# Performance work log

Measured on AMD Instinct MI355X. Metric: run time of the kernel, lower is better.

The kernel has to match this reference:

```python
import jax, jax.numpy as jnp
import numpy as np

B, CIN, H, W = 32, 256, 32, 32
DK, DV, HEADS, OUT = 128, 128, 8, 256
DKH = DK // HEADS
DVH = DV // HEADS


def _conv1x1(x, w, b):
    # x: [B,C,H,W], w: [O,C], b: [O]
    return jnp.einsum('bchw,oc->bohw', x, w) + b[None, :, None, None]


def setup_inputs() -> dict:
    key = jax.random.key(0)
    ks = jax.random.split(key, 7)
    s = 0.02
    return {
        'x': jax.random.normal(ks[0], (B, CIN, H, W), jnp.float32),
        'w_qkv': jax.random.normal(ks[1], (2 * DK + DV, CIN), jnp.float32) * s,
        'b_qkv': jnp.zeros((2 * DK + DV,), jnp.float32),
        'w_attn': jax.random.normal(ks[2], (DV, DV), jnp.float32) * s,
        'b_attn': jnp.zeros((DV,), jnp.float32),
        'w_out': jax.random.normal(ks[3], (OUT - DV, CIN), jnp.float32) * s,
        'b_out': jnp.zeros((OUT - DV,), jnp.float32),
    }


def reference(x, w_qkv, b_qkv, w_attn, b_attn, w_out, b_out):
    b = x.shape[0]
    N = H * W
    # parallel conv branch (kernel_size=1 so spatial dims match attention branch)
    conv_out = _conv1x1(x, w_out, b_out)  # [B, OUT-DV, H, W]
    # qkv projection
    qkv = _conv1x1(x, w_qkv, b_qkv)  # [B, 2*DK+DV, H, W]
    q, k, v = jnp.split(qkv, [DK, 2 * DK], axis=1)
    q = q.reshape(b, HEADS, DKH, N) * (DKH ** -0.5)
    k = k.reshape(b, HEADS, DKH, N)
    v = v.reshape(b, HEADS, DVH, N)
    # scaled dot-product attention over the N=H*W flattened positions
    logits = jnp.einsum('bhdq,bhdk->bhqk', q, k)  # [B,heads,N,N]
    weights = jax.nn.softmax(logits, axis=-1)
    attn = jnp.einsum('bhqk,bhdk->bhdq', weights, v)  # [B,heads,DVH,N]
    attn = attn.reshape(b, DV, H, W)
    attn = _conv1x1(attn, w_attn, b_attn)
    return jnp.concatenate([conv_out, attn], axis=1)
```

## Files before the change

kernel.cpp:

```cpp
#include <hip/hip_runtime.h>
#include <hip/hip_bf16.h>

#define BATCH 32
#define CIN   256
#define NPOS  1024
#define DKC   128
#define DVC   128
#define HEADS 8
#define OUTC  256

typedef __bf16 bf16x8 __attribute__((ext_vector_type(8)));
typedef __bf16 bf16x4 __attribute__((ext_vector_type(4)));
typedef float  f32x4  __attribute__((ext_vector_type(4)));
typedef float  f32x16 __attribute__((ext_vector_type(16)));
typedef unsigned u32x4 __attribute__((ext_vector_type(4)));

#define QSCALE 0.3606737602f

__device__ inline bf16x8 load8(const __bf16* p) {
    return *reinterpret_cast<const bf16x8*>(p);
}
__device__ inline f32x4 fzero4() {
    f32x4 z;
#pragma unroll
    for (int i = 0; i < 4; ++i) z[i] = 0.0f;
    return z;
}
__device__ inline float fexp2(float x) {
#if __has_builtin(__builtin_amdgcn_exp2f)
    return __builtin_amdgcn_exp2f(x);
#else
    return exp2f(x);
#endif
}

__global__ __launch_bounds__(256) void detect_dtype(const unsigned short* __restrict__ xraw,
                                                    int* __restrict__ flag) {
    __shared__ int s;
    if (threadIdx.x == 0) s = 0;
    __syncthreads();
    int cnt = 0;
#pragma unroll
    for (int j = 0; j < 64; ++j) {
        unsigned short u = xraw[threadIdx.x * 64 + j];
        unsigned int e = (u >> 7) & 0xFF;
        if (e >= 0x92) cnt++;
    }
    if (cnt) atomicAdd(&s, cnt);
    __syncthreads();
    if (threadIdx.x == 0) *flag = (s > 0) ? 1 : 0;
}

#define CV_WQKV 98304
#define CV_WOUT (CV_WQKV + 32768)
#define CV_BQKV (CV_WOUT + 384)
#define CV_BOUT (CV_BQKV + 128)
#define CV_WATT (CV_BOUT + 16384)
#define CV_BATT (CV_WATT + 128)
__global__ __launch_bounds__(256) void convert_all(
    const void* __restrict__ w_qkv, const void* __restrict__ b_qkv,
    const void* __restrict__ w_attn, const void* __restrict__ b_attn,
    const void* __restrict__ w_out, const void* __restrict__ b_out,
    __bf16* __restrict__ wcat, __bf16* __restrict__ bcat,
    __bf16* __restrict__ w_attnc, __bf16* __restrict__ b_attnc,
    const int* __restrict__ flag) {
    int i = blockIdx.x * 256 + threadIdx.x;
    const void* src; __bf16* dst; int j;
    if      (i < CV_WQKV) { src = w_qkv;  j = i;           dst = wcat + i; }
    else if (i < CV_WOUT) { src = w_out;  j = i - CV_WQKV; dst = wcat + i; }
    else if (i < CV_BQKV) { src = b_qkv;  j = i - CV_WOUT; dst = bcat + j; }
    else if (i < CV_BOUT) { src = b_out;  j = i - CV_BQKV; dst = bcat + 384 + j; }
    else if (i < CV_WATT) { src = w_attn; j = i - CV_BOUT; dst = w_attnc + j; }
    else if (i < CV_BATT) { src = b_attn; j = i - CV_WATT; dst = b_attnc + j; }
    else return;
    if (*flag) *dst = (__bf16)((const float*)src)[j];
    else       *dst = ((const __bf16*)src)[j];
}

__global__ __launch_bounds__(512, 4) void qkv_conv_gemm3(
    const void* __restrict__ xv,
    const __bf16* __restrict__ wcat,
    const __bf16* __restrict__ bcat,
    __bf16* __restrict__ q_ws,
    __bf16* __restrict__ k_ws,
    __bf16* __restrict__ v_ws,
    void* __restrict__ out,
    const int* __restrict__ flag)
{
    __shared__ __bf16 xs[64][264];
    bool isf32 = (*flag != 0);
    int b   = blockIdx.y;
    int n0  = blockIdx.x * 64;
    int t   = threadIdx.x;
    int nl  = t & 63, cb = t >> 6;

#pragma unroll
    for (int cs = 0; cs < 32; ++cs) {
        int c = cs * 8 + cb;
        size_t gi = ((size_t)b * CIN + c) * NPOS + n0 + nl;
        float v = isf32 ? ((const float*)xv)[gi] : (float)((const __bf16*)xv)[gi];
        xs[nl][c] = (__bf16)v;
    }
    __syncthreads();

    int wave = t >> 6;
    int lane = t & 63;
    int quad = lane >> 4, colid = lane & 15;
    int row0 = (wave >> 2) * 256 + (wave & 3) * 64;

    const __bf16* wp = wcat + (size_t)(row0 + colid) * CIN + quad * 8;

    f32x4 acc[4][4];
#pragma unroll
    for (int rt = 0; rt < 4; ++rt)
#pragma unroll
        for (int st = 0; st < 4; ++st) acc[rt][st] = fzero4();

#pragma unroll
    for (int k0 = 0; k0 < CIN; k0 += 32) {
        bf16x8 aA[4], bB[4];
#pragma unroll
        for (int rt = 0; rt < 4; ++rt)
            aA[rt] = load8(wp + (size_t)rt * 16 * CIN + k0);
#pragma unroll
        for (int st = 0; st < 4; ++st)
            bB[st] = *reinterpret_cast<const bf16x8*>(&xs[st * 16 + colid][k0 + quad * 8]);
#pragma unroll
        for (int rt = 0; rt < 4; ++rt)
#pragma unroll
            for (int st = 0; st < 4; ++st)
                acc[rt][st] = __builtin_amdgcn_mfma_f32_16x16x32_bf16(aA[rt], bB[st], acc[rt][st], 0, 0, 0);
    }

#pragma unroll
    for (int rt = 0; rt < 4; ++rt) {
        int obase = row0 + rt * 16;
        float bias[4];
#pragma unroll
        for (int r = 0; r < 4; ++r) bias[r] = (float)bcat[obase + quad * 4 + r];

        if (obase < DKC) {
            int h = obase >> 4;
            __bf16* qb = q_ws + (((size_t)b * HEADS + h) * NPOS + n0) * 16 + quad * 4;
#pragma unroll
            for (int st = 0; st < 4; ++st) {
                bf16x4 ov;
#pragma unroll
                for (int r = 0; r < 4; ++r)
                    ov[r] = (__bf16)((acc[rt][st][r] + bias[r]) * QSCALE);
                *reinterpret_cast<bf16x4*>(qb + (size_t)(st * 16 + colid) * 16) = ov;
            }
        } else if (obase < 2 * DKC) {
            int h = (obase - DKC) >> 4;
            __bf16* kb = k_ws + (((size_t)b * HEADS + h) * NPOS + n0) * 16 + quad * 4;
#pragma unroll
            for (int st = 0; st < 4; ++st) {
                bf16x4 ov;
#pragma unroll
                for (int r = 0; r < 4; ++r)
                    ov[r] = (__bf16)(acc[rt][st][r] + bias[r]);
                *reinterpret_cast<bf16x4*>(kb + (size_t)(st * 16 + colid) * 16) = ov;
            }
        } else if (obase < 384) {
            int h = (obase - 2 * DKC) >> 4;
            __bf16* vb = v_ws + (((size_t)b * HEADS + h) * 16 + quad * 4) * NPOS + n0 + colid;
#pragma unroll
            for (int r = 0; r < 4; ++r)
#pragma unroll
                for (int st = 0; st < 4; ++st)
                    vb[(size_t)r * NPOS + st * 16] = (__bf16)(acc[rt][st][r] + bias[r]);
        } else {
            int oc = obase - 384 + quad * 4;
#pragma unroll
            for (int r = 0; r < 4; ++r) {
                size_t ob = ((size_t)b * OUTC + oc + r) * NPOS + n0 + colid;
#pragma unroll
                for (int st = 0; st < 4; ++st) {
                    float v = acc[rt][st][r] + bias[r];
                    if (isf32) ((float*)out)[ob + st * 16] = v;
                    else       ((__bf16*)out)[ob + st * 16] = (__bf16)v;
                }
            }
        }
    }
}

#define OSTR 136
__global__ __launch_bounds__(512, 4) void attention_kernel(
    const __bf16* __restrict__ q_ws,
    const __bf16* __restrict__ k_ws,
    const __bf16* __restrict__ v_ws,
    const __bf16* __restrict__ w_attn,
    const __bf16* __restrict__ b_attn,
    void* __restrict__ out,
    const int* __restrict__ flag)
{
    __shared__ __align__(16) __bf16 olds[64][OSTR];
    int b    = blockIdx.x;
    int nq0  = blockIdx.y * 64;
    int wave = threadIdx.x >> 6;
    int lane = threadIdx.x & 63;
    int l5   = lane & 31, hi = lane >> 5;
    int h    = wave;
    int bh   = b * HEADS + h;

    const __bf16* qp = q_ws + (size_t)bh * NPOS * 16;
    const __bf16* kp = k_ws + (size_t)bh * NPOS * 16;
    const __bf16* vp = v_ws + (size_t)bh * 16 * NPOS;

    bf16x8 qB0 = load8(qp + (size_t)(nq0 + l5) * 16 + hi * 8);
    bf16x8 qB1 = load8(qp + (size_t)(nq0 + 32 + l5) * 16 + hi * 8);

    bf16x8 vA0, vA1;
#pragma unroll
    for (int i = 0; i < 8; ++i) { vA0[i] = (__bf16)1.0f; vA1[i] = (__bf16)1.0f; }
    const __bf16* vrow = vp + (size_t)l5 * NPOS + hi * 8;

    f32x16 zero16;
#pragma unroll
    for (int i = 0; i < 16; ++i) zero16[i] = 0.0f;
    f32x16 acc0 = zero16, acc1 = zero16;

    bf16x8 kA = load8(kp + (size_t)l5 * 16 + hi * 8);
    if (l5 < 16) {
        vA0 = load8(vrow);
        vA1 = load8(vrow + 16);
    }

#pragma unroll 2
    for (int nk0 = 0; nk0 < NPOS; nk0 += 32) {
        int nkn = (nk0 + 32) & (NPOS - 1);
        bf16x8 kA_n = load8(kp + (size_t)(nkn + l5) * 16 + hi * 8);
        bf16x8 vA0_n = vA0, vA1_n = vA1;
        if (l5 < 16) {
            vA0_n = load8(vrow + nkn);
            vA1_n = load8(vrow + nkn + 16);
        }
#pragma unroll
        for (int half = 0; half < 2; ++half) {
            f32x16 st = __builtin_amdgcn_mfma_f32_32x32x16_bf16(
                kA, half ? qB1 : qB0, zero16, 0, 0, 0);
            unsigned w[8];
#pragma unroll
            for (int m = 0; m < 4; ++m) {
                float e0 = fexp2(st[4 * m + 0]);
                float e1 = fexp2(st[4 * m + 1]);
                float e2 = fexp2(st[4 * m + 2]);
                float e3 = fexp2(st[4 * m + 3]);
                unsigned lo, hw;
                asm("v_cvt_pk_bf16_f32 %0, %1, %2" : "=v"(lo) : "v"(e0), "v"(e1));
                asm("v_cvt_pk_bf16_f32 %0, %1, %2" : "=v"(hw) : "v"(e2), "v"(e3));
                w[2 * m]     = lo;
                w[2 * m + 1] = hw;
            }
            asm("v_permlane32_swap_b32 %0, %1" : "+v"(w[0]), "+v"(w[2]));
            asm("v_permlane32_swap_b32 %0, %1" : "+v"(w[1]), "+v"(w[3]));
            asm("v_permlane32_swap_b32 %0, %1" : "+v"(w[4]), "+v"(w[6]));
            asm("v_permlane32_swap_b32 %0, %1" : "+v"(w[5]), "+v"(w[7]));
            u32x4 t1 = {w[0], w[1], w[2], w[3]};
            u32x4 t2 = {w[4], w[5], w[6], w[7]};
            bf16x8 pB1 = __builtin_bit_cast(bf16x8, t1);
            bf16x8 pB2 = __builtin_bit_cast(bf16x8, t2);
            if (half) {
                acc1 = __builtin_amdgcn_mfma_f32_32x32x16_bf16(vA0, pB1, acc1, 0, 0, 0);
                acc1 = __builtin_amdgcn_mfma_f32_32x32x16_bf16(vA1, pB2, acc1, 0, 0, 0);
            } else {
                acc0 = __builtin_amdgcn_mfma_f32_32x32x16_bf16(vA0, pB1, acc0, 0, 0, 0);
                acc0 = __builtin_amdgcn_mfma_f32_32x32x16_bf16(vA1, pB2, acc0, 0, 0, 0);
            }
        }
        kA = kA_n; vA0 = vA0_n; vA1 = vA1_n;
    }
#pragma unroll
    for (int half = 0; half < 2; ++half) {
        const f32x16& acc = half ? acc1 : acc0;
        float inv = 1.0f / acc[8];
        bf16x4 o0, o1;
#pragma unroll
        for (int r = 0; r < 4; ++r) {
            o0[r] = (__bf16)(acc[r] * inv);
            o1[r] = (__bf16)(acc[4 + r] * inv);
        }
        __bf16* ol = &olds[32 * half + l5][h * 16 + 4 * hi];
        *reinterpret_cast<bf16x4*>(ol)     = o0;
        *reinterpret_cast<bf16x4*>(ol + 8) = o1;
    }
    __syncthreads();

    int quad = lane >> 4, colid = lane & 15;
    int row0 = h * 16;
    f32x4 pacc[4];
#pragma unroll
    for (int st = 0; st < 4; ++st) pacc[st] = fzero4();
#pragma unroll
    for (int k0 = 0; k0 < DVC; k0 += 32) {
        bf16x8 a = load8(w_attn + (size_t)(row0 + colid) * DVC + k0 + quad * 8);
#pragma unroll
        for (int st = 0; st < 4; ++st) {
            bf16x8 bb = *reinterpret_cast<const bf16x8*>(&olds[st * 16 + colid][k0 + quad * 8]);
            pacc[st] = __builtin_amdgcn_mfma_f32_16x16x32_bf16(a, bb, pacc[st], 0, 0, 0);
        }
    }
    bool isf32 = (*flag != 0);
#pragma unroll
    for (int r = 0; r < 4; ++r) {
        int o = row0 + quad * 4 + r;
        float bias = (float)b_attn[o];
#pragma unroll
        for (int st = 0; st < 4; ++st) {
            int n = nq0 + st * 16 + colid;
            float v = pacc[st][r] + bias;
            size_t oi = ((size_t)b * OUTC + DVC + o) * NPOS + n;
            if (isf32) ((float*)out)[oi] = v;
            else       ((__bf16*)out)[oi] = (__bf16)v;
        }
    }
}

extern "C" void kernel_launch(void* const* d_in, const int* in_sizes, int n_in,
                              void* d_out, int out_size, void* d_ws, size_t ws_size,
                              hipStream_t stream) {
    const void* x      = d_in[0];
    const void* w_qkv  = d_in[1];
    const void* b_qkv  = d_in[2];
    const void* w_attn = d_in[3];
    const void* b_attn = d_in[4];
    const void* w_out  = d_in[5];
    const void* b_out  = d_in[6];

    char* ws = (char*)d_ws;
    int*    flag    = (int*)ws;
    __bf16* wcat    = (__bf16*)(ws + (1u << 20));
    __bf16* bcat    = (__bf16*)(ws + (3u << 19));
    __bf16* w_attnc = (__bf16*)(ws + (7u << 18));
    __bf16* b_attnc = (__bf16*)(ws + (1u << 21));
    __bf16* q_ws    = (__bf16*)(ws + (28u << 20));
    __bf16* k_ws    = (__bf16*)(ws + (36u << 20));
    __bf16* v_ws    = (__bf16*)(ws + (44u << 20));

    detect_dtype<<<1, 256, 0, stream>>>((const unsigned short*)x, flag);
    convert_all<<<(CV_BATT + 255) / 256, 256, 0, stream>>>(
        w_qkv, b_qkv, w_attn, b_attn, w_out, b_out,
        wcat, bcat, w_attnc, b_attnc, flag);

    qkv_conv_gemm3<<<dim3(NPOS / 64, BATCH), 512, 0, stream>>>(
        x, wcat, bcat, q_ws, k_ws, v_ws, d_out, flag);
    attention_kernel<<<dim3(BATCH, NPOS / 64), 512, 0, stream>>>(
        q_ws, k_ws, v_ws, w_attnc, b_attnc, d_out, flag);
}
```

Before: 164.7 us.

## Split GEMM output rows across grid z and halve attention query tile

The projection GEMM now runs with a 2-deep grid z, so each block computes 256 output rows with 32 rows per wave. It also prefetches the next weight fragment one k-step ahead. The attention kernel processes 32 queries per block instead of 64, doubling the block count, and both kernels raise launch bounds to 6 blocks per CU. The aim is more parallelism and occupancy. The cost is that the GEMM stages x into LDS twice, and the attention kernel rereads K/V twice as often with less MFMA work per exp and load.

Result: slower. 186.1 us (+13.0%).

```diff
diff --git a/kernel.cpp b/kernel.cpp
--- a/kernel.cpp
+++ b/kernel.cpp
@@ -77,7 +77,7 @@
     else       *dst = ((const __bf16*)src)[j];
 }
 
-__global__ __launch_bounds__(512, 4) void qkv_conv_gemm3(
+__global__ __launch_bounds__(512, 6) void qkv_conv_gemm4(
     const void* __restrict__ xv,
     const __bf16* __restrict__ wcat,
     const __bf16* __restrict__ bcat,
@@ -91,6 +91,7 @@
     bool isf32 = (*flag != 0);
     int b   = blockIdx.y;
     int n0  = blockIdx.x * 64;
+    int z   = blockIdx.z;
     int t   = threadIdx.x;
     int nl  = t & 63, cb = t >> 6;
 
@@ -106,34 +107,41 @@
     int wave = t >> 6;
     int lane = t & 63;
     int quad = lane >> 4, colid = lane & 15;
-    int row0 = (wave >> 2) * 256 + (wave & 3) * 64;
+    int row0 = z * 256 + wave * 32;
 
     const __bf16* wp = wcat + (size_t)(row0 + colid) * CIN + quad * 8;
 
-    f32x4 acc[4][4];
-#pragma unroll
-    for (int rt = 0; rt < 4; ++rt)
+    f32x4 acc[2][4];
+#pragma unroll
+    for (int rt = 0; rt < 2; ++rt)
 #pragma unroll
         for (int st = 0; st < 4; ++st) acc[rt][st] = fzero4();
 
-#pragma unroll
-    for (int k0 = 0; k0 < CIN; k0 += 32) {
-        bf16x8 aA[4], bB[4];
-#pragma unroll
-        for (int rt = 0; rt < 4; ++rt)
-            aA[rt] = load8(wp + (size_t)rt * 16 * CIN + k0);
+    bf16x8 aA[2];
+#pragma unroll
+    for (int rt = 0; rt < 2; ++rt)
+        aA[rt] = load8(wp + (size_t)(rt * 16) * CIN);
+
+#pragma unroll
+    for (int k = 0; k < 8; ++k) {
+        int k0 = k * 32;
+        bf16x8 bB[4];
 #pragma unroll
         for (int st = 0; st < 4; ++st)
             bB[st] = *reinterpret_cast<const bf16x8*>(&xs[st * 16 + colid][k0 + quad * 8]);
 #pragma unroll
-        for (int rt = 0; rt < 4; ++rt)
+        for (int rt = 0; rt < 2; ++rt) {
+            bf16x8 a = aA[rt];
+            if (k < 7)
+                aA[rt] = load8(wp + (size_t)(rt * 16) * CIN + k0 + 32);
 #pragma unroll
             for (int st = 0; st < 4; ++st)
-                acc[rt][st] = __builtin_amdgcn_mfma_f32_16x16x32_bf16(aA[rt], bB[st], acc[rt][st], 0, 0, 0);
-    }
-
-#pragma unroll
-    for (int rt = 0; rt < 4; ++rt) {
+                acc[rt][st] = __builtin_amdgcn_mfma_f32_16x16x32_bf16(a, bB[st], acc[rt][st], 0, 0, 0);
+        }
+    }
+
+#pragma unroll
+    for (int rt = 0; rt < 2; ++rt) {
         int obase = row0 + rt * 16;
         float bias[4];
 #pragma unroll
@@ -186,7 +194,7 @@
 }
 
 #define OSTR 136
-__global__ __launch_bounds__(512, 4) void attention_kernel(
+__global__ __launch_bounds__(512, 6) void attention_kernel(
     const __bf16* __restrict__ q_ws,
     const __bf16* __restrict__ k_ws,
     const __bf16* __restrict__ v_ws,
@@ -195,9 +203,9 @@
     void* __restrict__ out,
     const int* __restrict__ flag)
 {
-    __shared__ __align__(16) __bf16 olds[64][OSTR];
+    __shared__ __align__(16) __bf16 olds[32][OSTR];
     int b    = blockIdx.x;
-    int nq0  = blockIdx.y * 64;
+    int nq0  = blockIdx.y * 32;
     int wave = threadIdx.x >> 6;
     int lane = threadIdx.x & 63;
     int l5   = lane & 31, hi = lane >> 5;
@@ -208,8 +216,7 @@
     const __bf16* kp = k_ws + (size_t)bh * NPOS * 16;
     const __bf16* vp = v_ws + (size_t)bh * 16 * NPOS;
 
-    bf16x8 qB0 = load8(qp + (size_t)(nq0 + l5) * 16 + hi * 8);
-    bf16x8 qB1 = load8(qp + (size_t)(nq0 + 32 + l5) * 16 + hi * 8);
+    bf16x8 qB = load8(qp + (size_t)(nq0 + l5) * 16 + hi * 8);
 
     bf16x8 vA0, vA1;
 #pragma unroll
@@ -219,7 +226,7 @@
     f32x16 zero16;
 #pragma unroll
     for (int i = 0; i < 16; ++i) zero16[i] = 0.0f;
-    f32x16 acc0 = zero16, acc1 = zero16;
+    f32x16 acc = zero16;
 
     bf16x8 kA = load8(kp + (size_t)l5 * 16 + hi * 8);
     if (l5 < 16) {
@@ -236,67 +243,54 @@
             vA0_n = load8(vrow + nkn);
             vA1_n = load8(vrow + nkn + 16);
         }
-#pragma unroll
-        for (int half = 0; half < 2; ++half) {
-            f32x16 st = __builtin_amdgcn_mfma_f32_32x32x16_bf16(
-                kA, half ? qB1 : qB0, zero16, 0, 0, 0);
-            unsigned w[8];
-#pragma unroll
-            for (int m = 0; m < 4; ++m) {
-                float e0 = fexp2(st[4 * m + 0]);
-                float e1 = fexp2(st[4 * m + 1]);
-                float e2 = fexp2(st[4 * m + 2]);
-                float e3 = fexp2(st[4 * m + 3]);
-                unsigned lo, hw;
-                asm("v_cvt_pk_bf16_f32 %0, %1, %2" : "=v"(lo) : "v"(e0), "v"(e1));
-                asm("v_cvt_pk_bf16_f32 %0, %1, %2" : "=v"(hw) : "v"(e2), "v"(e3));
-                w[2 * m]     = lo;
-                w[2 * m + 1] = hw;
-            }
-            asm("v_permlane32_swap_b32 %0, %1" : "+v"(w[0]), "+v"(w[2]));
-            asm("v_permlane32_swap_b32 %0, %1" : "+v"(w[1]), "+v"(w[3]));
-            asm("v_permlane32_swap_b32 %0, %1" : "+v"(w[4]), "+v"(w[6]));
-            asm("v_permlane32_swap_b32 %0, %1" : "+v"(w[5]), "+v"(w[7]));
-            u32x4 t1 = {w[0], w[1], w[2], w[3]};
-            u32x4 t2 = {w[4], w[5], w[6], w[7]};
-            bf16x8 pB1 = __builtin_bit_cast(bf16x8, t1);
-            bf16x8 pB2 = __builtin_bit_cast(bf16x8, t2);
-            if (half) {
-                acc1 = __builtin_amdgcn_mfma_f32_32x32x16_bf16(vA0, pB1, acc1, 0, 0, 0);
-                acc1 = __builtin_amdgcn_mfma_f32_32x32x16_bf16(vA1, pB2, acc1, 0, 0, 0);
-            } else {
-                acc0 = __builtin_amdgcn_mfma_f32_32x32x16_bf16(vA0, pB1, acc0, 0, 0, 0);
-                acc0 = __builtin_amdgcn_mfma_f32_32x32x16_bf16(vA1, pB2, acc0, 0, 0, 0);
-            }
-        }
+        f32x16 st = __builtin_amdgcn_mfma_f32_32x32x16_bf16(kA, qB, zero16, 0, 0, 0);
+        unsigned w[8];
+#pragma unroll
+        for (int m = 0; m < 4; ++m) {
+            float e0 = fexp2(st[4 * m + 0]);
+            float e1 = fexp2(st[4 * m + 1]);
+            float e2 = fexp2(st[4 * m + 2]);
+            float e3 = fexp2(st[4 * m + 3]);
+            unsigned lo, hw;
+            asm("v_cvt_pk_bf16_f32 %0, %1, %2" : "=v"(lo) : "v"(e0), "v"(e1));
+            asm("v_cvt_pk_bf16_f32 %0, %1, %2" : "=v"(hw) : "v"(e2), "v"(e3));
+            w[2 * m]     = lo;
+            w[2 * m + 1] = hw;
+        }
+        asm("v_permlane32_swap_b32 %0, %1" : "+v"(w[0]), "+v"(w[2]));
+        asm("v_permlane32_swap_b32 %0, %1" : "+v"(w[1]), "+v"(w[3]));
+        asm("v_permlane32_swap_b32 %0, %1" : "+v"(w[4]), "+v"(w[6]));
+        asm("v_permlane32_swap_b32 %0, %1" : "+v"(w[5]), "+v"(w[7]));
+        u32x4 t1 = {w[0], w[1], w[2], w[3]};
+        u32x4 t2 = {w[4], w[5], w[6], w[7]};
+        bf16x8 pB1 = __builtin_bit_cast(bf16x8, t1);
+        bf16x8 pB2 = __builtin_bit_cast(bf16x8, t2);
+        acc = __builtin_amdgcn_mfma_f32_32x32x16_bf16(vA0, pB1, acc, 0, 0, 0);
+        acc = __builtin_amdgcn_mfma_f32_32x32x16_bf16(vA1, pB2, acc, 0, 0, 0);
         kA = kA_n; vA0 = vA0_n; vA1 = vA1_n;
     }
-#pragma unroll
-    for (int half = 0; half < 2; ++half) {
-        const f32x16& acc = half ? acc1 : acc0;
-        float inv = 1.0f / acc[8];
-        bf16x4 o0, o1;
-#pragma unroll
-        for (int r = 0; r < 4; ++r) {
-            o0[r] = (__bf16)(acc[r] * inv);
-            o1[r] = (__bf16)(acc[4 + r] * inv);
-        }
-        __bf16* ol = &olds[32 * half + l5][h * 16 + 4 * hi];
-        *reinterpret_cast<bf16x4*>(ol)     = o0;
-        *reinterpret_cast<bf16x4*>(ol + 8) = o1;
-    }
+    float inv = 1.0f / acc[8];
+    bf16x4 o0, o1;
+#pragma unroll
+    for (int r = 0; r < 4; ++r) {
+        o0[r] = (__bf16)(acc[r] * inv);
+        o1[r] = (__bf16)(acc[4 + r] * inv);
+    }
+    __bf16* ol = &olds[l5][h * 16 + 4 * hi];
+    *reinterpret_cast<bf16x4*>(ol)     = o0;
+    *reinterpret_cast<bf16x4*>(ol + 8) = o1;
     __syncthreads();
 
     int quad = lane >> 4, colid = lane & 15;
     int row0 = h * 16;
-    f32x4 pacc[4];
-#pragma unroll
-    for (int st = 0; st < 4; ++st) pacc[st] = fzero4();
+    f32x4 pacc[2];
+#pragma unroll
+    for (int st = 0; st < 2; ++st) pacc[st] = fzero4();
 #pragma unroll
     for (int k0 = 0; k0 < DVC; k0 += 32) {
         bf16x8 a = load8(w_attn + (size_t)(row0 + colid) * DVC + k0 + quad * 8);
 #pragma unroll
-        for (int st = 0; st < 4; ++st) {
+        for (int st = 0; st < 2; ++st) {
             bf16x8 bb = *reinterpret_cast<const bf16x8*>(&olds[st * 16 + colid][k0 + quad * 8]);
             pacc[st] = __builtin_amdgcn_mfma_f32_16x16x32_bf16(a, bb, pacc[st], 0, 0, 0);
         }
@@ -307,7 +301,7 @@
         int o = row0 + quad * 4 + r;
         float bias = (float)b_attn[o];
 #pragma unroll
-        for (int st = 0; st < 4; ++st) {
+        for (int st = 0; st < 2; ++st) {
             int n = nq0 + st * 16 + colid;
             float v = pacc[st][r] + bias;
             size_t oi = ((size_t)b * OUTC + DVC + o) * NPOS + n;
@@ -343,8 +337,8 @@
         w_qkv, b_qkv, w_attn, b_attn, w_out, b_out,
         wcat, bcat, w_attnc, b_attnc, flag);
 
-    qkv_conv_gemm3<<<dim3(NPOS / 64, BATCH), 512, 0, stream>>>(
+    qkv_conv_gemm4<<<dim3(NPOS / 64, BATCH, 2), 512, 0, stream>>>(
         x, wcat, bcat, q_ws, k_ws, v_ws, d_out, flag);
-    attention_kernel<<<dim3(BATCH, NPOS / 64), 512, 0, stream>>>(
+    attention_kernel<<<dim3(BATCH, NPOS / 32), 512, 0, stream>>>(
         q_ws, k_ws, v_ws, w_attnc, b_attnc, d_out, flag);
 }
```
